# Optimization experiments

Hardware: AMD Instinct MI355X
Metric: run time of the kernel (lower is better)

The kernel has to match this reference:

```python
import jax, jax.numpy as jnp
import numpy as np

N, E = 50000, 800000
IN_CH, HID, OUT_CH = 128, 256, 40
L, R = 3, 16
EPS = 1e-12


def setup_inputs() -> dict:
    key = jax.random.key(0)
    ks = jax.random.split(key, 16)
    s = 0.05
    return {
        'x': jax.random.normal(ks[0], (N, IN_CH), jnp.float32),
        'edge_index': jax.random.randint(ks[1], (2, E), 0, N, dtype=jnp.int64),
        'W_in': jax.random.normal(ks[2], (IN_CH, HID), jnp.float32) * s,
        'b_in': jnp.zeros((HID,), jnp.float32),
        'centers': jax.random.normal(ks[3], (L, R, HID), jnp.float32),
        'log_sigma': jnp.zeros((L, R, HID), jnp.float32),
        'W_rule': jax.random.normal(ks[4], (L, R, HID, HID), jnp.float32) * s,
        'b_rule': jnp.zeros((L, R, HID), jnp.float32),
        'W_self': jax.random.normal(ks[5], (L, HID, HID), jnp.float32) * s,
        'b_self': jnp.zeros((L, HID), jnp.float32),
        'gamma': jnp.ones((L, HID), jnp.float32),
        'beta': jnp.zeros((L, HID), jnp.float32),
        'W_h1': jax.random.normal(ks[6], (HID, HID // 2), jnp.float32) * s,
        'b_h1': jnp.zeros((HID // 2,), jnp.float32),
        'W_h2': jax.random.normal(ks[7], (HID // 2, OUT_CH), jnp.float32) * s,
        'b_h2': jnp.zeros((OUT_CH,), jnp.float32),
    }


def membership(h, c, log_s):
    # Gaussian rule firing, expanded to matmuls to avoid [N,R,H] distance tensor
    inv_s2 = jnp.exp(-2.0 * log_s)                         # [R,H]
    d = (h * h) @ inv_s2.T - 2.0 * (h @ (c * inv_s2).T) \
        + jnp.sum(c * c * inv_s2, axis=-1)                 # [N,R]
    firing = jnp.exp(-0.5 * d)
    return firing / (jnp.sum(firing, axis=-1, keepdims=True) + EPS)


def fmpl(h, src, dst, c, log_s, W_r, b_r, W_s, b_s):
    n = h.shape[0]
    deg = jax.ops.segment_sum(jnp.ones(src.shape[0], h.dtype), dst, num_segments=n)
    agg = jax.ops.segment_sum(h[src], dst, num_segments=n) / jnp.clip(deg, 1.0)[:, None]
    mu = membership(h, c, log_s)                           # [N,R]
    per_rule = jnp.einsum('ni,rio->nro', agg, W_r) + b_r[None]  # [N,R,H]
    fuzzy = jnp.einsum('nr,nro->no', mu, per_rule)
    return h @ W_s + b_s + fuzzy


def batchnorm(x, g, b, eps=1e-5):
    m = jnp.mean(x, axis=0)
    v = jnp.var(x, axis=0)
    return (x - m) * jax.lax.rsqrt(v + eps) * g + b


def reference(x, edge_index, W_in, b_in, centers, log_sigma, W_rule, b_rule,
              W_self, b_self, gamma, beta, W_h1, b_h1, W_h2, b_h2):
    src, dst = edge_index[0], edge_index[1]
    h = jax.nn.relu(x @ W_in + b_in)                       # dropout = identity (eval)
    for l in range(L):
        h_new = fmpl(h, src, dst, centers[l], log_sigma[l], W_rule[l], b_rule[l],
                     W_self[l], b_self[l])
        h_new = jax.nn.relu(batchnorm(h_new, gamma[l], beta[l]))
        h = h + h_new
    logits = jax.nn.relu(h @ W_h1 + b_h1) @ W_h2 + b_h2
    return jax.nn.softmax(logits, axis=-1)
```

## Files before the change

### kernel.cpp

```cpp
#include <hip/hip_runtime.h>
#include <hip/hip_fp16.h>
#include <cstdint>
#include <cstddef>

using u16 = unsigned short;
using u32 = unsigned int;

typedef _Float16 half8 __attribute__((ext_vector_type(8)));
typedef float f32x4 __attribute__((ext_vector_type(4)));

#define MF(a, b, c) __builtin_amdgcn_mfma_f32_16x16x32_f16((a), (b), (c), 0, 0, 0)

static inline int cdiv(int a, int b) { return (a + b - 1) / b; }


__global__ void prep_k(const float* __restrict__ Wr,
                       const float* __restrict__ Ws, const float* __restrict__ br,
                       const float* __restrict__ W_in, const float* __restrict__ W_h1,
                       const float* __restrict__ W_h2,
                       const float* __restrict__ centers, const float* __restrict__ logsig,
                       u16* __restrict__ wcat,
                       u16* __restrict__ winp, u16* __restrict__ wh1p,
                       u16* __restrict__ wh2p,
                       u16* __restrict__ pcB, float* __restrict__ pccc,
                       int* __restrict__ zerobase, int nzero,
                       int Z, int Wb) {
    const int bid = blockIdx.x;
    const int tid = threadIdx.x;
    if (bid < Z) {
        int i = bid * 256 + tid;
        if (i < nzero) zerobase[i] = 0;
        return;
    }
    if (bid < Z + Wb) {
        size_t t = (size_t)(bid - Z) * 256 + tid;
        const size_t PL = 552u * 256u * 8u;
        int l = (int)(t / PL);
        size_t rem = t - (size_t)l * PL;
        int kp = (int)(rem >> 11);
        int o = (int)((rem >> 3) & 255);
        int e = (int)(rem & 7);
        int k = kp * 8 + e;
        float v;
        if (k < 4096)      v = Wr[((((size_t)l * 16 + (k >> 8)) * 256) + (k & 255)) * 256 + o];
        else if (k < 4352) v = Ws[(((size_t)l * 256) + (k - 4096)) * 256 + o];
        else if (k < 4368) v = br[(((size_t)l * 16) + (k - 4352)) * 256 + o];
        else               v = 0.f;
        union { u16 u; _Float16 h; } c; c.h = (_Float16)v;
        wcat[t] = c.u;
        return;
    }
    if (bid < Z + Wb + 128) {
        size_t t = (size_t)(bid - Z - Wb) * 256 + tid;
        int e = (int)(t & 7), o = (int)((t >> 3) & 255);
        int kp = (int)(t >> 11);
        union { u16 u; _Float16 h; } c; c.h = (_Float16)W_in[(size_t)(kp * 8 + e) * 256 + o];
        winp[t] = c.u;
        return;
    }
    if (bid < Z + Wb + 256) {
        size_t t = (size_t)(bid - Z - Wb - 128) * 256 + tid;
        int e = (int)(t & 7), o = (int)((t >> 3) & 127);
        int kp = (int)(t >> 10);
        union { u16 u; _Float16 h; } c; c.h = (_Float16)W_h1[(size_t)(kp * 8 + e) * 128 + o];
        wh1p[t] = c.u;
        return;
    }
    if (bid < Z + Wb + 256 + 24) {
        int t = (bid - Z - Wb - 256) * 256 + tid;
        int e = t & 7, col = (t >> 3) % 48, p = t / 384;
        int k = p * 8 + e;
        float v = (col < 40) ? W_h2[(size_t)k * 40 + col] : 0.f;
        union { u16 u; _Float16 h; } c; c.h = (_Float16)v;
        wh2p[t] = c.u;
        return;
    }
    {
        int lr = bid - (Z + Wb + 256 + 24);
        size_t idx = (size_t)lr * 256 + tid;
        float ls = logsig[idx];
        float inv = expf(-2.f * ls);
        float c = centers[idx];
        union { u16 u; _Float16 h; } c1, c2;
        c1.h = (_Float16)inv;
        c2.h = (_Float16)(-2.f * c * inv);
        pcB[(size_t)lr * 512 + tid] = c1.u;
        pcB[(size_t)lr * 512 + 256 + tid] = c2.u;
        __shared__ float sm[256];
        sm[tid] = c * c * inv;
        __syncthreads();
        for (int s = 128; s > 0; s >>= 1) { if (tid < s) sm[tid] += sm[tid + s]; __syncthreads(); }
        if (tid == 0) pccc[lr] = sm[0];
    }
}


__launch_bounds__(256, 4)
__global__ void csr_agg_g(const int* __restrict__ src, const int* __restrict__ dst,
                          int* __restrict__ deg, int* __restrict__ indptr,
                          int* __restrict__ cursor, float* __restrict__ deginv,
                          int* __restrict__ ssrc, int* __restrict__ csrctr,
                          const int* __restrict__ bflag, int* __restrict__ done,
                          const u16* __restrict__ h16, u16* __restrict__ agg16,
                          int E, int n) {
    if (bflag[511] == 0) return;
    const int tid = threadIdx.x;
    if (*done == 0) {
        auto gbar = [&](int id) {
            __threadfence();
            __syncthreads();
            if (tid == 0) {
                atomicAdd(csrctr, 1);
                while (atomicAdd(csrctr, 0) < 256 * id) __builtin_amdgcn_s_sleep(2);
            }
            __syncthreads();
        };
        for (int e = blockIdx.x * 256 + tid; e < E; e += 256 * 256)
            atomicAdd(&deg[dst[e]], 1);
        gbar(1);
        if (blockIdx.x == 0) {
            const int chunk = (n + 255) >> 8;
            int s0 = tid * chunk, s1 = s0 + chunk; if (s1 > n) s1 = n; if (s0 > n) s0 = n;
            int tot = 0;
            for (int i = s0; i < s1; ++i) tot += atomicAdd(&deg[i], 0);
            __shared__ int sm[256];
            sm[tid] = tot; __syncthreads();
            for (int off = 1; off < 256; off <<= 1) {
                int t = (tid >= off) ? sm[tid - off] : 0;
                __syncthreads(); sm[tid] += t; __syncthreads();
            }
            int base = sm[tid] - tot;
            for (int i = s0; i < s1; ++i) {
                int d = atomicAdd(&deg[i], 0);
                indptr[i] = base; cursor[i] = base;
                deginv[i] = 1.f / (float)(d > 1 ? d : 1);
                base += d;
            }
            if (tid == 255) indptr[n] = sm[255];
        }
        gbar(2);
        for (int e = blockIdx.x * 256 + tid; e < E; e += 256 * 256) {
            int d = dst[e];
            int pos = atomicAdd(&cursor[d], 1);
            ssrc[pos] = src[e];
        }
        gbar(3);
        if (blockIdx.x == 0 && tid == 0) *done = 1;
    }
    int lane = tid & 63, wave = tid >> 6;
    for (int node = blockIdx.x * 4 + wave; node < n; node += 256 * 4) {
        if (bflag[node >> 7] == 0) continue;
        int j0 = indptr[node], j1 = indptr[node + 1];
        float a0 = 0, a1 = 0, a2 = 0, a3 = 0;
        for (int j = j0; j < j1; ++j) {
            int sN = ssrc[j];
            union { uint2 u; _Float16 h[4]; } hv;
            hv.u = *(const uint2*)(h16 + (size_t)sN * 256 + lane * 4);
            a0 += (float)hv.h[0]; a1 += (float)hv.h[1];
            a2 += (float)hv.h[2]; a3 += (float)hv.h[3];
        }
        float di = deginv[node];
        union { uint2 u; _Float16 h[4]; } o;
        o.h[0] = (_Float16)(a0 * di); o.h[1] = (_Float16)(a1 * di);
        o.h[2] = (_Float16)(a2 * di); o.h[3] = (_Float16)(a3 * di);
        *(uint2*)(agg16 + (size_t)node * 256 + lane * 4) = o.u;
    }
}


template <int MODE, int NCHUNK>
__launch_bounds__(256, 2)
__global__ void gemm_mn(const u16* __restrict__ A, const u16* __restrict__ A2,
                        const u16* __restrict__ MU, const u16* __restrict__ Bp,
                        const float* __restrict__ bias, const int* __restrict__ bflag,
                        u16* __restrict__ outH, float* __restrict__ bnsum,
                        const u16* __restrict__ pcB, const float* __restrict__ pccc,
                        u16* __restrict__ mu16, int* __restrict__ bflagN,
                        int nrows) {
    __shared__ __align__(16) u16 lds[24576];
    __shared__ float bnbuf[2048];
    u16* lA = lds;
    u16* lB = lds + 8192;
    const int tid = threadIdx.x;
    const int row0 = blockIdx.x * 128;
    const int lane = tid & 63;
    const int q = lane >> 4, mm = lane & 15;
    const int wave = tid >> 6;

    f32x4 acc[2][16];
#pragma unroll
    for (int i = 0; i < 2; ++i)
#pragma unroll
        for (int j = 0; j < 16; ++j) acc[i][j] = (f32x4){0.f, 0.f, 0.f, 0.f};

    int cb = 0, cbEnd = NCHUNK;
    if (MODE == 1 && bflag[blockIdx.x] == 0) { cb = 64; cbEnd = 68; }

    for (; cb < cbEnd; ++cb) {
#pragma unroll
        for (int it = 0; it < 8; ++it) {
            int idx = it * 256 + tid;
            int p = idx >> 8, col = idx & 255;
            uint4 v = *(const uint4*)(Bp + (((size_t)(cb * 8 + p)) * 256 + col) * 8);
            *(uint4*)(lB + (size_t)idx * 8) = v;
        }
#pragma unroll
        for (int it = 0; it < 4; ++it) {
            int idx = it * 256 + tid;
            int p = idx >> 7, row = idx & 127;
            int grow = row0 + row; if (grow >= nrows) grow = nrows - 1;
            uint4 v;
            if (MODE == 0) {
                const float* xr = (const float*)A + (size_t)grow * 128 + cb * 64 + (p << 3);
                float4 f0 = *(const float4*)xr;
                float4 f1 = *(const float4*)(xr + 4);
                union { uint4 u4; _Float16 h[8]; } cv;
                cv.h[0] = (_Float16)f0.x; cv.h[1] = (_Float16)f0.y;
                cv.h[2] = (_Float16)f0.z; cv.h[3] = (_Float16)f0.w;
                cv.h[4] = (_Float16)f1.x; cv.h[5] = (_Float16)f1.y;
                cv.h[6] = (_Float16)f1.z; cv.h[7] = (_Float16)f1.w;
                v = cv.u4;
            } else {
                if (cb < 64) {
                    int r = cb >> 2;
                    int i0 = ((cb & 3) << 6) + (p << 3);
                    v = *(const uint4*)(A + (size_t)grow * 256 + i0);
                    union { u16 u; _Float16 h; } mu; mu.u = MU[(size_t)grow * 16 + r];
                    union { uint4 u4; _Float16 h[8]; } wv; wv.u4 = v;
#pragma unroll
                    for (int j = 0; j < 8; ++j) wv.h[j] = wv.h[j] * mu.h;
                    v = wv.u4;
                } else if (cb < 68) {
                    int i0 = ((cb - 64) << 6) + (p << 3);
                    v = *(const uint4*)(A2 + (size_t)grow * 256 + i0);
                } else {
                    int j0 = p << 3;
                    if (j0 < 16) v = *(const uint4*)(MU + (size_t)grow * 16 + j0);
                    else v = (uint4){0, 0, 0, 0};
                }
            }
            *(uint4*)(lA + (size_t)idx * 8) = v;
        }
        __syncthreads();
#pragma unroll
        for (int kc = 0; kc < 2; ++kc) {
            int pp = kc * 4 + q;
            half8 af0 = *(const half8*)(lA + ((size_t)pp * 128 + wave * 32 + mm) * 8);
            half8 af1 = *(const half8*)(lA + ((size_t)pp * 128 + wave * 32 + 16 + mm) * 8);
#pragma unroll
            for (int nt = 0; nt < 16; ++nt) {
                half8 bf = *(const half8*)(lB + ((size_t)pp * 256 + nt * 16 + mm) * 8);
                acc[0][nt] = MF(af0, bf, acc[0][nt]);
                acc[1][nt] = MF(af1, bf, acc[1][nt]);
            }
        }
        __syncthreads();
    }

    int nr = nrows - row0; if (nr > 128) nr = 128;

    if (MODE == 1) {
#pragma unroll
        for (int nt = 0; nt < 16; ++nt) {
            int cl = nt * 16 + mm;
            float bb = bias[cl];
            float s = 0.f, ss = 0.f;
#pragma unroll
            for (int mt = 0; mt < 2; ++mt) {
#pragma unroll
                for (int r = 0; r < 4; ++r) {
                    int row = wave * 32 + mt * 16 + q * 4 + r;
                    float v = acc[mt][nt][r] + bb;
                    if (row < nr) { s += v; ss += v * v; }
                }
            }
            s += __shfl_xor(s, 16);  s += __shfl_xor(s, 32);
            ss += __shfl_xor(ss, 16); ss += __shfl_xor(ss, 32);
            if (q == 0) {
                bnbuf[(wave * 256 + cl) * 2 + 0] = s;
                bnbuf[(wave * 256 + cl) * 2 + 1] = ss;
            }
        }
        __syncthreads();
        {
            float s  = bnbuf[tid * 2]     + bnbuf[(256 + tid) * 2]
                     + bnbuf[(512 + tid) * 2] + bnbuf[(768 + tid) * 2];
            float ss = bnbuf[tid * 2 + 1] + bnbuf[(256 + tid) * 2 + 1]
                     + bnbuf[(512 + tid) * 2 + 1] + bnbuf[(768 + tid) * 2 + 1];
            atomicAdd(&bnsum[tid], s);
            atomicAdd(&bnsum[256 + tid], ss);
        }
    }

    f32x4 macc0 = (f32x4){0.f, 0.f, 0.f, 0.f};
    f32x4 macc1 = (f32x4){0.f, 0.f, 0.f, 0.f};
#pragma unroll
    for (int h = 0; h < 2; ++h) {
        __syncthreads();
#pragma unroll
        for (int nt = 0; nt < 8; ++nt) {
            int cl = h * 128 + nt * 16 + mm;
            float bb = bias[cl];
#pragma unroll
            for (int mt = 0; mt < 2; ++mt) {
#pragma unroll
                for (int r = 0; r < 4; ++r) {
                    int row = wave * 32 + mt * 16 + q * 4 + r;
                    float v = acc[mt][h * 8 + nt][r] + bb;
                    if (MODE == 0) v = fmaxf(v, 0.f);
                    union { u16 u; _Float16 hh; } cc; cc.hh = (_Float16)v;
                    lds[row * 136 + nt * 16 + mm] = cc.u;
                }
            }
        }
        __syncthreads();
#pragma unroll
        for (int it = 0; it < 8; ++it) {
            int idx = it * 256 + tid;
            int row = idx >> 4, cp = idx & 15;
            if (row < nr) {
                uint4 v = *(const uint4*)(lds + row * 136 + cp * 8);
                *(uint4*)(outH + (size_t)(row0 + row) * 256 + h * 128 + cp * 8) = v;
            }
        }
        if (MODE == 0) {
            const u16* brow = pcB + (size_t)mm * 512;
#pragma unroll
            for (int it2 = 0; it2 < 4; ++it2) {
                int lk = it2 * 32 + q * 8;
                half8 b1 = *(const half8*)(brow + h * 128 + lk);
                half8 b2 = *(const half8*)(brow + 256 + h * 128 + lk);
                half8 a0 = *(const half8*)(lds + ((size_t)(wave * 32 + mm)) * 136 + lk);
                half8 a1 = *(const half8*)(lds + ((size_t)(wave * 32 + 16 + mm)) * 136 + lk);
                macc0 = MF(a0 * a0, b1, macc0);
                macc0 = MF(a0, b2, macc0);
                macc1 = MF(a1 * a1, b1, macc1);
                macc1 = MF(a1, b2, macc1);
            }
        }
    }

    if (MODE == 0) {
        float cc = pccc[mm];
        bool any = false;
#pragma unroll
        for (int g = 0; g < 2; ++g) {
            f32x4 macc = g ? macc1 : macc0;
#pragma unroll
            for (int r = 0; r < 4; ++r) {
                float d = macc[r] + cc;
                float f = expf(-0.5f * d);
                float s = f;
                s += __shfl_xor(s, 1); s += __shfl_xor(s, 2);
                s += __shfl_xor(s, 4); s += __shfl_xor(s, 8);
                int node = row0 + (wave * 2 + g) * 16 + q * 4 + r;
                if (node < nrows) {
                    union { u16 u; _Float16 hh; } c2;
                    c2.hh = (_Float16)(f / (s + 1e-12f));
                    mu16[(size_t)node * 16 + mm] = c2.u;
                    if (c2.u != 0) any = true;
                }
            }
        }
        if (__any(any) && lane == 0) {
            atomicOr(&bflagN[blockIdx.x], 1);
            atomicOr(&bflagN[511], 1);
        }
    }
}


template <int TAIL>
__launch_bounds__(256)
__global__ void upd_k(const u16* __restrict__ pre16, const float* __restrict__ bnsum,
                      const float* __restrict__ gamma, const float* __restrict__ beta,
                      u16* __restrict__ h16,
                      const u16* __restrict__ pcB, const float* __restrict__ pccc,
                      u16* __restrict__ mu16, int* __restrict__ bflag,
                      const u16* __restrict__ wh1p, const float* __restrict__ bh1,
                      const u16* __restrict__ wh2p, const float* __restrict__ bh2,
                      float* __restrict__ outF, int n) {
    const int tid = threadIdx.x;
    __shared__ float l_ab[512];
    __shared__ __align__(16) u16 qt[4][2176];
    {
        float su = bnsum[tid];
        float sq = bnsum[256 + tid];
        float invn = 1.f / (float)n;
        float m = su * invn;
        float al = gamma[tid] * rsqrtf(sq * invn - m * m + 1e-5f);
        l_ab[tid] = al;
        l_ab[256 + tid] = beta[tid] - m * al;
    }
    __syncthreads();

    const int lane = tid & 63, wave = tid >> 6;
    const int q = lane >> 4, mm = lane & 15;
    const int n0 = (blockIdx.x * 4 + wave) * 16;
    if (n0 >= n) return;
    const int node = n0 + mm;
    const bool valid = node < n;
    const int nodeC = valid ? node : n - 1;
    const size_t base = (size_t)nodeC * 256 + q * 8;

    half8 v16[8];
#pragma unroll
    for (int b = 0; b < 8; ++b) {
        int c = b * 32 + q * 8;
        float4 alA = *(const float4*)(l_ab + c);
        float4 alB = *(const float4*)(l_ab + c + 4);
        float4 shA = *(const float4*)(l_ab + 256 + c);
        float4 shB = *(const float4*)(l_ab + 256 + c + 4);
        float aarr[8] = {alA.x, alA.y, alA.z, alA.w, alB.x, alB.y, alB.z, alB.w};
        float harr[8] = {shA.x, shA.y, shA.z, shA.w, shB.x, shB.y, shB.z, shB.w};
        union { uint4 u; _Float16 hh[8]; } p, hv, o;
        p.u  = *(const uint4*)(pre16 + base + b * 32);
        hv.u = *(const uint4*)(h16 + base + b * 32);
#pragma unroll
        for (int j = 0; j < 8; ++j) {
            float v = (float)hv.hh[j] + fmaxf((float)p.hh[j] * aarr[j] + harr[j], 0.f);
            o.hh[j] = (_Float16)v;
        }
        if (TAIL == 1 && valid) *(uint4*)(h16 + base + b * 32) = o.u;
        v16[b] = *(half8*)&o;
    }

    if (TAIL == 1) {
        const u16* brow = pcB + (size_t)mm * 512;
        f32x4 acc = (f32x4){0.f, 0.f, 0.f, 0.f};
#pragma unroll
        for (int it = 0; it < 16; ++it) {
            half8 a = v16[it & 7];
            if (it < 8) a = a * a;
            half8 bb = *(const half8*)(brow + it * 32 + q * 8);
            acc = MF(a, bb, acc);
        }
        float cc = pccc[mm];
        bool any = false;
#pragma unroll
        for (int r = 0; r < 4; ++r) {
            float d = acc[r] + cc;
            float f = expf(-0.5f * d);
            float s = f;
            s += __shfl_xor(s, 1); s += __shfl_xor(s, 2);
            s += __shfl_xor(s, 4); s += __shfl_xor(s, 8);
            int nd = n0 + q * 4 + r;
            if (nd < n) {
                union { u16 u; _Float16 h; } c2;
                c2.h = (_Float16)(f / (s + 1e-12f));
                mu16[(size_t)nd * 16 + mm] = c2.u;
                if (c2.u != 0) any = true;
            }
        }
        if (__any(any) && lane == 0) {
            atomicOr(&bflag[n0 >> 7], 1);
            atomicOr(&bflag[511], 1);
        }
    }

    if (TAIL == 2) {
        u16* qw = qt[wave];
        f32x4 hq[8];
#pragma unroll
        for (int j = 0; j < 8; ++j) hq[j] = (f32x4){0.f, 0.f, 0.f, 0.f};
#pragma unroll
        for (int b = 0; b < 8; ++b) {
            half8 a = v16[b];
            const u16* bp = wh1p + ((size_t)((b * 4 + q) * 128) + mm) * 8;
#pragma unroll
            for (int nt = 0; nt < 8; ++nt) {
                half8 bf = *(const half8*)(bp + nt * 128);
                hq[nt] = MF(a, bf, hq[nt]);
            }
        }
#pragma unroll
        for (int nt = 0; nt < 8; ++nt) {
            int cl = nt * 16 + mm;
            float bb = bh1[cl];
#pragma unroll
            for (int r = 0; r < 4; ++r) {
                float v = fmaxf(hq[nt][r] + bb, 0.f);
                union { u16 u; _Float16 h; } cc; cc.h = (_Float16)v;
                qw[(q * 4 + r) * 136 + cl] = cc.u;
            }
        }
        const bool c2ok = (mm < 8);
        float b0 = bh2[mm], b1 = bh2[16 + mm];
        float b2 = c2ok ? bh2[32 + mm] : 0.f;
        f32x4 hacc[3];
#pragma unroll
        for (int t = 0; t < 3; ++t) hacc[t] = (f32x4){0.f, 0.f, 0.f, 0.f};
#pragma unroll
        for (int c = 0; c < 4; ++c) {
            half8 a = *(const half8*)(qw + (size_t)mm * 136 + c * 32 + q * 8);
#pragma unroll
            for (int t = 0; t < 3; ++t) {
                half8 b = *(const half8*)(wh2p + ((size_t)(c * 4 + q) * 48 + t * 16 + mm) * 8);
                hacc[t] = MF(a, b, hacc[t]);
            }
        }
#pragma unroll
        for (int r = 0; r < 4; ++r) {
            int nd = n0 + q * 4 + r;
            float v0 = hacc[0][r] + b0;
            float v1 = hacc[1][r] + b1;
            float v2 = c2ok ? (hacc[2][r] + b2) : -3e38f;
            float m = fmaxf(fmaxf(v0, v1), v2);
            m = fmaxf(m, __shfl_xor(m, 1)); m = fmaxf(m, __shfl_xor(m, 2));
            m = fmaxf(m, __shfl_xor(m, 4)); m = fmaxf(m, __shfl_xor(m, 8));
            float e0 = expf(v0 - m), e1 = expf(v1 - m);
            float e2 = c2ok ? expf(v2 - m) : 0.f;
            float s = e0 + e1 + e2;
            s += __shfl_xor(s, 1); s += __shfl_xor(s, 2);
            s += __shfl_xor(s, 4); s += __shfl_xor(s, 8);
            float is = 1.f / s;
            if (nd < n) {
                float* op = outF + (size_t)nd * 40;
                op[mm] = e0 * is;
                op[16 + mm] = e1 * is;
                if (c2ok) op[32 + mm] = e2 * is;
            }
        }
    }
}


extern "C" void kernel_launch(void* const* d_in, const int* in_sizes, int n_in,
                              void* d_out, int out_size, void* d_ws, size_t ws_size,
                              hipStream_t stream) {
    const float* x       = (const float*)d_in[0];
    const int*   ei      = (const int*)d_in[1];
    const float* W_in    = (const float*)d_in[2];
    const float* b_in    = (const float*)d_in[3];
    const float* centers = (const float*)d_in[4];
    const float* logsig  = (const float*)d_in[5];
    const float* W_rule  = (const float*)d_in[6];
    const float* b_rule  = (const float*)d_in[7];
    const float* W_self  = (const float*)d_in[8];
    const float* b_self  = (const float*)d_in[9];
    const float* gamma   = (const float*)d_in[10];
    const float* beta    = (const float*)d_in[11];
    const float* W_h1    = (const float*)d_in[12];
    const float* b_h1    = (const float*)d_in[13];
    const float* W_h2    = (const float*)d_in[14];
    const float* b_h2    = (const float*)d_in[15];

    const int N = in_sizes[0] / 128;
    const int E = in_sizes[1] / 2;
    const int* e_src = ei;
    const int* e_dst = ei + E;

    char* w = (char*)d_ws;
    size_t off = 0;
    auto alloc = [&](size_t bytes) -> void* {
        void* p = w + off;
        off = (off + bytes + 255) & ~(size_t)255;
        return p;
    };

    const int gx = cdiv(N, 128);

    u16*   h16    = (u16*)  alloc((size_t)N * 256 * 2);
    u16*   pre16  = (u16*)  alloc((size_t)N * 256 * 2);
    u16*   agg16  = (u16*)  alloc((size_t)N * 256 * 2);
    u16*   mu16   = (u16*)  alloc((size_t)N * 16 * 2);
    u16*   wcat   = (u16*)  alloc((size_t)3 * 552 * 256 * 8 * 2);
    u16*   winp   = (u16*)  alloc((size_t)16 * 256 * 8 * 2);
    u16*   wh1p   = (u16*)  alloc((size_t)32 * 128 * 8 * 2);
    u16*   wh2p   = (u16*)  alloc((size_t)16 * 48 * 8 * 2);
    u16*   pcB    = (u16*)  alloc((size_t)48 * 512 * 2);
    float* pccc   = (float*)alloc((size_t)48 * 4);
    int*   indptr = (int*)  alloc((size_t)(N + 1) * 4);
    int*   cursor = (int*)  alloc((size_t)N * 4);
    float* deginv = (float*)alloc((size_t)N * 4);
    int*   ssrc   = (int*)  alloc((size_t)E * 4);
    const int nzero = N + 3 * 512 + 3 * 512 + 16;
    int*   zerob  = (int*)  alloc((size_t)nzero * 4);
    int*   deg    = zerob;
    int*   bflagA = zerob + N;
    float* bnsumA = (float*)(zerob + N + 3 * 512);
    int*   misc   = zerob + N + 3 * 512 + 3 * 512;
    int*   done   = misc;
    int*   csrctr = misc + 1;

    const int Z = cdiv(nzero, 256);
    const int Wb = 3 * 552 * 256 * 8 / 256;
    const int prep_grid = Z + Wb + 128 + 128 + 24 + 48;

    prep_k<<<prep_grid, 256, 0, stream>>>(W_rule, W_self, b_rule, W_in, W_h1, W_h2,
                                          centers, logsig, wcat, winp, wh1p, wh2p,
                                          pcB, pccc, zerob, nzero, Z, Wb);

    gemm_mn<0, 2><<<gx, 256, 0, stream>>>((const u16*)x, nullptr, nullptr, winp,
                                          b_in, nullptr, h16, nullptr,
                                          pcB, pccc, mu16, bflagA, N);

    for (int l = 0; l < 3; ++l) {
        int* bf = bflagA + l * 512;
        float* bns = bnsumA + l * 512;
        csr_agg_g<<<256, 256, 0, stream>>>(e_src, e_dst, deg, indptr, cursor, deginv,
                                           ssrc, csrctr, bf, done, h16, agg16, E, N);
        gemm_mn<1, 69><<<gx, 256, 0, stream>>>(agg16, h16, mu16,
                                               wcat + (size_t)l * 552 * 256 * 8,
                                               b_self + l * 256, bf, pre16, bns,
                                               nullptr, nullptr, nullptr, nullptr, N);
        if (l < 2) {
            upd_k<1><<<cdiv(N, 64), 256, 0, stream>>>(pre16, bns, gamma + l * 256,
                                                      beta + l * 256, h16,
                                                      pcB + (size_t)(l + 1) * 16 * 512,
                                                      pccc + (l + 1) * 16, mu16,
                                                      bflagA + (l + 1) * 512,
                                                      nullptr, nullptr, nullptr, nullptr,
                                                      nullptr, N);
        } else {
            upd_k<2><<<cdiv(N, 64), 256, 0, stream>>>(pre16, bns, gamma + l * 256,
                                                      beta + l * 256, h16,
                                                      nullptr, nullptr, nullptr, nullptr,
                                                      wh1p, b_h1, wh2p, b_h2,
                                                      (float*)d_out, N);
        }
    }
}
```

Baseline: 293.6 us.

## Fuse CSR build and aggregation into layer GEMM, convert weights on the fly

Drops the separate CSR/aggregation kernel. Its work moves into the front of the layer GEMM kernel: the edge histogram, scan and scatter run once behind a grid barrier, then each block aggregates its own 128 rows before running the matrix product on them. The fp16 weight prepacking in the prep kernel is also removed, so the GEMM now loads fp32 W_rule, W_self, b_rule and W_in directly and converts them to fp16 while staging each B tile. This saves launches and a large weight-packing pass. In exchange, every block rereads fp32 weights at twice the bytes and does extra conversions in the inner loop. The grid barrier also relies on all GEMM blocks being resident on the GPU at the same time.

New measurement: 340.6 us. 1.16x slower.

```diff
diff --git a/kernel.cpp b/kernel.cpp
--- a/kernel.cpp
+++ b/kernel.cpp
@@ -14,17 +14,11 @@
 static inline int cdiv(int a, int b) { return (a + b - 1) / b; }
 
 
-__global__ void prep_k(const float* __restrict__ Wr,
-                       const float* __restrict__ Ws, const float* __restrict__ br,
-                       const float* __restrict__ W_in, const float* __restrict__ W_h1,
-                       const float* __restrict__ W_h2,
+__global__ void prep_k(const float* __restrict__ W_h1, const float* __restrict__ W_h2,
                        const float* __restrict__ centers, const float* __restrict__ logsig,
-                       u16* __restrict__ wcat,
-                       u16* __restrict__ winp, u16* __restrict__ wh1p,
-                       u16* __restrict__ wh2p,
+                       u16* __restrict__ wh1p, u16* __restrict__ wh2p,
                        u16* __restrict__ pcB, float* __restrict__ pccc,
-                       int* __restrict__ zerobase, int nzero,
-                       int Z, int Wb) {
+                       int* __restrict__ zerobase, int nzero, int Z) {
     const int bid = blockIdx.x;
     const int tid = threadIdx.x;
     if (bid < Z) {
@@ -32,42 +26,16 @@
         if (i < nzero) zerobase[i] = 0;
         return;
     }
-    if (bid < Z + Wb) {
+    if (bid < Z + 128) {
         size_t t = (size_t)(bid - Z) * 256 + tid;
-        const size_t PL = 552u * 256u * 8u;
-        int l = (int)(t / PL);
-        size_t rem = t - (size_t)l * PL;
-        int kp = (int)(rem >> 11);
-        int o = (int)((rem >> 3) & 255);
-        int e = (int)(rem & 7);
-        int k = kp * 8 + e;
-        float v;
-        if (k < 4096)      v = Wr[((((size_t)l * 16 + (k >> 8)) * 256) + (k & 255)) * 256 + o];
-        else if (k < 4352) v = Ws[(((size_t)l * 256) + (k - 4096)) * 256 + o];
-        else if (k < 4368) v = br[(((size_t)l * 16) + (k - 4352)) * 256 + o];
-        else               v = 0.f;
-        union { u16 u; _Float16 h; } c; c.h = (_Float16)v;
-        wcat[t] = c.u;
-        return;
-    }
-    if (bid < Z + Wb + 128) {
-        size_t t = (size_t)(bid - Z - Wb) * 256 + tid;
-        int e = (int)(t & 7), o = (int)((t >> 3) & 255);
-        int kp = (int)(t >> 11);
-        union { u16 u; _Float16 h; } c; c.h = (_Float16)W_in[(size_t)(kp * 8 + e) * 256 + o];
-        winp[t] = c.u;
-        return;
-    }
-    if (bid < Z + Wb + 256) {
-        size_t t = (size_t)(bid - Z - Wb - 128) * 256 + tid;
         int e = (int)(t & 7), o = (int)((t >> 3) & 127);
         int kp = (int)(t >> 10);
         union { u16 u; _Float16 h; } c; c.h = (_Float16)W_h1[(size_t)(kp * 8 + e) * 128 + o];
         wh1p[t] = c.u;
         return;
     }
-    if (bid < Z + Wb + 256 + 24) {
-        int t = (bid - Z - Wb - 256) * 256 + tid;
+    if (bid < Z + 128 + 24) {
+        int t = (bid - Z - 128) * 256 + tid;
         int e = t & 7, col = (t >> 3) % 48, p = t / 384;
         int k = p * 8 + e;
         float v = (col < 40) ? W_h2[(size_t)k * 40 + col] : 0.f;
@@ -76,7 +44,7 @@
         return;
     }
     {
-        int lr = bid - (Z + Wb + 256 + 24);
+        int lr = bid - (Z + 128 + 24);
         size_t idx = (size_t)lr * 256 + tid;
         float ls = logsig[idx];
         float inv = expf(-2.f * ls);
@@ -95,97 +63,101 @@
 }
 
 
-__launch_bounds__(256, 4)
-__global__ void csr_agg_g(const int* __restrict__ src, const int* __restrict__ dst,
-                          int* __restrict__ deg, int* __restrict__ indptr,
-                          int* __restrict__ cursor, float* __restrict__ deginv,
-                          int* __restrict__ ssrc, int* __restrict__ csrctr,
-                          const int* __restrict__ bflag, int* __restrict__ done,
-                          const u16* __restrict__ h16, u16* __restrict__ agg16,
-                          int E, int n) {
-    if (bflag[511] == 0) return;
-    const int tid = threadIdx.x;
-    if (*done == 0) {
-        auto gbar = [&](int id) {
-            __threadfence();
-            __syncthreads();
-            if (tid == 0) {
-                atomicAdd(csrctr, 1);
-                while (atomicAdd(csrctr, 0) < 256 * id) __builtin_amdgcn_s_sleep(2);
-            }
-            __syncthreads();
-        };
-        for (int e = blockIdx.x * 256 + tid; e < E; e += 256 * 256)
-            atomicAdd(&deg[dst[e]], 1);
-        gbar(1);
-        if (blockIdx.x == 0) {
-            const int chunk = (n + 255) >> 8;
-            int s0 = tid * chunk, s1 = s0 + chunk; if (s1 > n) s1 = n; if (s0 > n) s0 = n;
-            int tot = 0;
-            for (int i = s0; i < s1; ++i) tot += atomicAdd(&deg[i], 0);
-            __shared__ int sm[256];
-            sm[tid] = tot; __syncthreads();
-            for (int off = 1; off < 256; off <<= 1) {
-                int t = (tid >= off) ? sm[tid - off] : 0;
-                __syncthreads(); sm[tid] += t; __syncthreads();
-            }
-            int base = sm[tid] - tot;
-            for (int i = s0; i < s1; ++i) {
-                int d = atomicAdd(&deg[i], 0);
-                indptr[i] = base; cursor[i] = base;
-                deginv[i] = 1.f / (float)(d > 1 ? d : 1);
-                base += d;
-            }
-            if (tid == 255) indptr[n] = sm[255];
-        }
-        gbar(2);
-        for (int e = blockIdx.x * 256 + tid; e < E; e += 256 * 256) {
-            int d = dst[e];
-            int pos = atomicAdd(&cursor[d], 1);
-            ssrc[pos] = src[e];
-        }
-        gbar(3);
-        if (blockIdx.x == 0 && tid == 0) *done = 1;
-    }
-    int lane = tid & 63, wave = tid >> 6;
-    for (int node = blockIdx.x * 4 + wave; node < n; node += 256 * 4) {
-        if (bflag[node >> 7] == 0) continue;
-        int j0 = indptr[node], j1 = indptr[node + 1];
-        float a0 = 0, a1 = 0, a2 = 0, a3 = 0;
-        for (int j = j0; j < j1; ++j) {
-            int sN = ssrc[j];
-            union { uint2 u; _Float16 h[4]; } hv;
-            hv.u = *(const uint2*)(h16 + (size_t)sN * 256 + lane * 4);
-            a0 += (float)hv.h[0]; a1 += (float)hv.h[1];
-            a2 += (float)hv.h[2]; a3 += (float)hv.h[3];
-        }
-        float di = deginv[node];
-        union { uint2 u; _Float16 h[4]; } o;
-        o.h[0] = (_Float16)(a0 * di); o.h[1] = (_Float16)(a1 * di);
-        o.h[2] = (_Float16)(a2 * di); o.h[3] = (_Float16)(a3 * di);
-        *(uint2*)(agg16 + (size_t)node * 256 + lane * 4) = o.u;
-    }
-}
-
-
 template <int MODE, int NCHUNK>
 __launch_bounds__(256, 2)
-__global__ void gemm_mn(const u16* __restrict__ A, const u16* __restrict__ A2,
-                        const u16* __restrict__ MU, const u16* __restrict__ Bp,
-                        const float* __restrict__ bias, const int* __restrict__ bflag,
-                        u16* __restrict__ outH, float* __restrict__ bnsum,
-                        const u16* __restrict__ pcB, const float* __restrict__ pccc,
-                        u16* __restrict__ mu16, int* __restrict__ bflagN,
-                        int nrows) {
+__global__ void gemm_f(const float* __restrict__ xf, const float* __restrict__ Wr,
+                       const float* __restrict__ Ws, const float* __restrict__ brl,
+                       int layer,
+                       u16* __restrict__ agg, const u16* __restrict__ hg,
+                       const u16* __restrict__ MU,
+                       const float* __restrict__ bias, const int* __restrict__ bflag,
+                       u16* __restrict__ outH, float* __restrict__ bnsum,
+                       const u16* __restrict__ pcB, const float* __restrict__ pccc,
+                       u16* __restrict__ mu16o, int* __restrict__ bflagN,
+                       const int* __restrict__ esrc, const int* __restrict__ edst,
+                       int* __restrict__ deg, int* __restrict__ indptr,
+                       int* __restrict__ cursor, float* __restrict__ deginv,
+                       int* __restrict__ ssrc, int* __restrict__ csrctr,
+                       int* __restrict__ done, int E, int nrows) {
     __shared__ __align__(16) u16 lds[24576];
-    __shared__ float bnbuf[2048];
+    __shared__ int ssm[256];
     u16* lA = lds;
     u16* lB = lds + 8192;
-    const int tid = threadIdx.x;
-    const int row0 = blockIdx.x * 128;
+    const int tid = threadIdx.x, bid = blockIdx.x;
+    const int row0 = bid * 128;
     const int lane = tid & 63;
     const int q = lane >> 4, mm = lane & 15;
     const int wave = tid >> 6;
+    int nr = nrows - row0; if (nr > 128) nr = 128;
+
+    if (MODE == 1 && bflag[511] != 0) {
+        int bseq = 0;
+        auto gbar = [&]() {
+            __threadfence();
+            __syncthreads();
+            ++bseq;
+            if (tid == 0) {
+                atomicAdd(csrctr, 1);
+                while (atomicAdd(csrctr, 0) < (int)gridDim.x * bseq)
+                    __builtin_amdgcn_s_sleep(2);
+            }
+            __syncthreads();
+        };
+        if (*done == 0) {
+            for (int e = bid * 256 + tid; e < E; e += (int)gridDim.x * 256)
+                atomicAdd(&deg[edst[e]], 1);
+            gbar();
+            if (bid == 0) {
+                const int n = nrows;
+                const int chunk = (n + 255) >> 8;
+                int s0 = tid * chunk, s1 = s0 + chunk;
+                if (s1 > n) s1 = n; if (s0 > n) s0 = n;
+                int tot = 0;
+                for (int i = s0; i < s1; ++i) tot += atomicAdd(&deg[i], 0);
+                ssm[tid] = tot; __syncthreads();
+                for (int off = 1; off < 256; off <<= 1) {
+                    int t = (tid >= off) ? ssm[tid - off] : 0;
+                    __syncthreads(); ssm[tid] += t; __syncthreads();
+                }
+                int base = ssm[tid] - tot;
+                for (int i = s0; i < s1; ++i) {
+                    int d = atomicAdd(&deg[i], 0);
+                    indptr[i] = base; cursor[i] = base;
+                    deginv[i] = 1.f / (float)(d > 1 ? d : 1);
+                    base += d;
+                }
+                if (tid == 255) indptr[nrows] = ssm[255];
+            }
+            gbar();
+            for (int e = bid * 256 + tid; e < E; e += (int)gridDim.x * 256) {
+                int d = edst[e];
+                int pos = atomicAdd(&cursor[d], 1);
+                ssrc[pos] = esrc[e];
+            }
+            gbar();
+            if (bid == 0 && tid == 0) *done = 1;
+        }
+        if (bflag[bid] != 0) {
+            for (int node = row0 + wave; node < row0 + 128 && node < nrows; node += 4) {
+                int j0 = indptr[node], j1 = indptr[node + 1];
+                float a0 = 0, a1 = 0, a2 = 0, a3 = 0;
+                for (int j = j0; j < j1; ++j) {
+                    int sN = ssrc[j];
+                    union { uint2 u; _Float16 h[4]; } hv;
+                    hv.u = *(const uint2*)(hg + (size_t)sN * 256 + lane * 4);
+                    a0 += (float)hv.h[0]; a1 += (float)hv.h[1];
+                    a2 += (float)hv.h[2]; a3 += (float)hv.h[3];
+                }
+                float di = deginv[node];
+                union { uint2 u; _Float16 h[4]; } o;
+                o.h[0] = (_Float16)(a0 * di); o.h[1] = (_Float16)(a1 * di);
+                o.h[2] = (_Float16)(a2 * di); o.h[3] = (_Float16)(a3 * di);
+                *(uint2*)(agg + (size_t)node * 256 + lane * 4) = o.u;
+            }
+        }
+        __threadfence_block();
+        __syncthreads();
+    }
 
     f32x4 acc[2][16];
 #pragma unroll
@@ -194,15 +166,43 @@
         for (int j = 0; j < 16; ++j) acc[i][j] = (f32x4){0.f, 0.f, 0.f, 0.f};
 
     int cb = 0, cbEnd = NCHUNK;
-    if (MODE == 1 && bflag[blockIdx.x] == 0) { cb = 64; cbEnd = 68; }
+    if (MODE == 1 && bflag[bid] == 0) { cb = 64; cbEnd = 68; }
 
     for (; cb < cbEnd; ++cb) {
 #pragma unroll
         for (int it = 0; it < 8; ++it) {
             int idx = it * 256 + tid;
             int p = idx >> 8, col = idx & 255;
-            uint4 v = *(const uint4*)(Bp + (((size_t)(cb * 8 + p)) * 256 + col) * 8);
-            *(uint4*)(lB + (size_t)idx * 8) = v;
+            int kb = cb * 64 + p * 8;
+            union { uint4 u4; _Float16 h[8]; } cv;
+            if (MODE == 0) {
+#pragma unroll
+                for (int e = 0; e < 8; ++e)
+                    cv.h[e] = (_Float16)xf[0], cv.h[e] = (_Float16)0.f;
+#pragma unroll
+                for (int e = 0; e < 8; ++e)
+                    cv.h[e] = (_Float16)Ws[(size_t)(kb + e) * 256 + col];
+            } else {
+                if (kb < 4096) {
+#pragma unroll
+                    for (int e = 0; e < 8; ++e) {
+                        int k = kb + e;
+                        cv.h[e] = (_Float16)Wr[((((size_t)layer * 16 + (k >> 8)) * 256)
+                                                + (k & 255)) * 256 + col];
+                    }
+                } else if (kb < 4352) {
+#pragma unroll
+                    for (int e = 0; e < 8; ++e)
+                        cv.h[e] = (_Float16)Ws[(((size_t)layer * 256) + (kb + e - 4096)) * 256 + col];
+                } else if (kb < 4368) {
+#pragma unroll
+                    for (int e = 0; e < 8; ++e)
+                        cv.h[e] = (_Float16)brl[(((size_t)layer * 16) + (kb + e - 4352)) * 256 + col];
+                } else {
+                    cv.u4 = (uint4){0, 0, 0, 0};
+                }
+            }
+            *(uint4*)(lB + (size_t)idx * 8) = cv.u4;
         }
 #pragma unroll
         for (int it = 0; it < 4; ++it) {
@@ -211,7 +211,7 @@
             int grow = row0 + row; if (grow >= nrows) grow = nrows - 1;
             uint4 v;
             if (MODE == 0) {
-                const float* xr = (const float*)A + (size_t)grow * 128 + cb * 64 + (p << 3);
+                const float* xr = xf + (size_t)grow * 128 + cb * 64 + (p << 3);
                 float4 f0 = *(const float4*)xr;
                 float4 f1 = *(const float4*)(xr + 4);
                 union { uint4 u4; _Float16 h[8]; } cv;
@@ -224,7 +224,7 @@
                 if (cb < 64) {
                     int r = cb >> 2;
                     int i0 = ((cb & 3) << 6) + (p << 3);
-                    v = *(const uint4*)(A + (size_t)grow * 256 + i0);
+                    v = *(const uint4*)(agg + (size_t)grow * 256 + i0);
                     union { u16 u; _Float16 h; } mu; mu.u = MU[(size_t)grow * 16 + r];
                     union { uint4 u4; _Float16 h[8]; } wv; wv.u4 = v;
 #pragma unroll
@@ -232,7 +232,7 @@
                     v = wv.u4;
                 } else if (cb < 68) {
                     int i0 = ((cb - 64) << 6) + (p << 3);
-                    v = *(const uint4*)(A2 + (size_t)grow * 256 + i0);
+                    v = *(const uint4*)(hg + (size_t)grow * 256 + i0);
                 } else {
                     int j0 = p << 3;
                     if (j0 < 16) v = *(const uint4*)(MU + (size_t)grow * 16 + j0);
@@ -257,9 +257,8 @@
         __syncthreads();
     }
 
-    int nr = nrows - row0; if (nr > 128) nr = 128;
-
     if (MODE == 1) {
+        float* bnbuf = (float*)lds;
 #pragma unroll
         for (int nt = 0; nt < 16; ++nt) {
             int cl = nt * 16 + mm;
@@ -357,13 +356,13 @@
                 if (node < nrows) {
                     union { u16 u; _Float16 hh; } c2;
                     c2.hh = (_Float16)(f / (s + 1e-12f));
-                    mu16[(size_t)node * 16 + mm] = c2.u;
+                    mu16o[(size_t)node * 16 + mm] = c2.u;
                     if (c2.u != 0) any = true;
                 }
             }
         }
         if (__any(any) && lane == 0) {
-            atomicOr(&bflagN[blockIdx.x], 1);
+            atomicOr(&bflagN[bid], 1);
             atomicOr(&bflagN[511], 1);
         }
     }
@@ -564,8 +563,6 @@
     u16*   pre16  = (u16*)  alloc((size_t)N * 256 * 2);
     u16*   agg16  = (u16*)  alloc((size_t)N * 256 * 2);
     u16*   mu16   = (u16*)  alloc((size_t)N * 16 * 2);
-    u16*   wcat   = (u16*)  alloc((size_t)3 * 552 * 256 * 8 * 2);
-    u16*   winp   = (u16*)  alloc((size_t)16 * 256 * 8 * 2);
     u16*   wh1p   = (u16*)  alloc((size_t)32 * 128 * 8 * 2);
     u16*   wh2p   = (u16*)  alloc((size_t)16 * 48 * 8 * 2);
     u16*   pcB    = (u16*)  alloc((size_t)48 * 512 * 2);
@@ -584,26 +581,28 @@
     int*   csrctr = misc + 1;
 
     const int Z = cdiv(nzero, 256);
-    const int Wb = 3 * 552 * 256 * 8 / 256;
-    const int prep_grid = Z + Wb + 128 + 128 + 24 + 48;
-
-    prep_k<<<prep_grid, 256, 0, stream>>>(W_rule, W_self, b_rule, W_in, W_h1, W_h2,
-                                          centers, logsig, wcat, winp, wh1p, wh2p,
-                                          pcB, pccc, zerob, nzero, Z, Wb);
-
-    gemm_mn<0, 2><<<gx, 256, 0, stream>>>((const u16*)x, nullptr, nullptr, winp,
-                                          b_in, nullptr, h16, nullptr,
-                                          pcB, pccc, mu16, bflagA, N);
+    const int prep_grid = Z + 128 + 24 + 48;
+
+    prep_k<<<prep_grid, 256, 0, stream>>>(W_h1, W_h2, centers, logsig,
+                                          wh1p, wh2p, pcB, pccc, zerob, nzero, Z);
+
+    gemm_f<0, 2><<<gx, 256, 0, stream>>>(x, nullptr, W_in, nullptr, 0,
+                                         nullptr, nullptr, nullptr,
+                                         b_in, nullptr, h16, nullptr,
+                                         pcB, pccc, mu16, bflagA,
+                                         nullptr, nullptr, nullptr, nullptr,
+                                         nullptr, nullptr, nullptr, nullptr,
+                                         nullptr, 0, N);
 
     for (int l = 0; l < 3; ++l) {
         int* bf = bflagA + l * 512;
         float* bns = bnsumA + l * 512;
-        csr_agg_g<<<256, 256, 0, stream>>>(e_src, e_dst, deg, indptr, cursor, deginv,
-                                           ssrc, csrctr, bf, done, h16, agg16, E, N);
-        gemm_mn<1, 69><<<gx, 256, 0, stream>>>(agg16, h16, mu16,
-                                               wcat + (size_t)l * 552 * 256 * 8,
-                                               b_self + l * 256, bf, pre16, bns,
-                                               nullptr, nullptr, nullptr, nullptr, N);
+        gemm_f<1, 69><<<gx, 256, 0, stream>>>(nullptr, W_rule, W_self, b_rule, l,
+                                              agg16, h16, mu16,
+                                              b_self + l * 256, bf, pre16, bns,
+                                              nullptr, nullptr, nullptr, nullptr,
+                                              e_src, e_dst, deg, indptr, cursor,
+                                              deginv, ssrc, csrctr, done, E, N);
         if (l < 2) {
             upd_k<1><<<cdiv(N, 64), 256, 0, stream>>>(pre16, bns, gamma + l * 256,
                                                       beta + l * 256, h16,
```

## Fuse CSR build and neighbor aggregation into the rule GEMM kernel

Applied to the files above, without the earlier changes.

Removes the separate csr_agg_g launch and performs the CSR construction (with grid barriers) and mean aggregation inside gemm_mn MODE 1. Each block now aggregates its own 128 rows into agg16 before running the GEMM on them, which saves one launch per layer and keeps the aggregated rows cache-warm. The grid barrier now spans gx blocks (about 391) instead of 256. All blocks must be co-resident for the spin barrier to work, and with launch_bounds(256,2) plus large LDS use this is a deadlock risk. Aggregation parallelism is also limited to 4 waves per block.

After: 289.2 us. Within noise of the previous version (-1.5%).

```diff
diff --git a/kernel.cpp b/kernel.cpp
--- a/kernel.cpp
+++ b/kernel.cpp
@@ -95,79 +95,6 @@
 }
 
 
-__launch_bounds__(256, 4)
-__global__ void csr_agg_g(const int* __restrict__ src, const int* __restrict__ dst,
-                          int* __restrict__ deg, int* __restrict__ indptr,
-                          int* __restrict__ cursor, float* __restrict__ deginv,
-                          int* __restrict__ ssrc, int* __restrict__ csrctr,
-                          const int* __restrict__ bflag, int* __restrict__ done,
-                          const u16* __restrict__ h16, u16* __restrict__ agg16,
-                          int E, int n) {
-    if (bflag[511] == 0) return;
-    const int tid = threadIdx.x;
-    if (*done == 0) {
-        auto gbar = [&](int id) {
-            __threadfence();
-            __syncthreads();
-            if (tid == 0) {
-                atomicAdd(csrctr, 1);
-                while (atomicAdd(csrctr, 0) < 256 * id) __builtin_amdgcn_s_sleep(2);
-            }
-            __syncthreads();
-        };
-        for (int e = blockIdx.x * 256 + tid; e < E; e += 256 * 256)
-            atomicAdd(&deg[dst[e]], 1);
-        gbar(1);
-        if (blockIdx.x == 0) {
-            const int chunk = (n + 255) >> 8;
-            int s0 = tid * chunk, s1 = s0 + chunk; if (s1 > n) s1 = n; if (s0 > n) s0 = n;
-            int tot = 0;
-            for (int i = s0; i < s1; ++i) tot += atomicAdd(&deg[i], 0);
-            __shared__ int sm[256];
-            sm[tid] = tot; __syncthreads();
-            for (int off = 1; off < 256; off <<= 1) {
-                int t = (tid >= off) ? sm[tid - off] : 0;
-                __syncthreads(); sm[tid] += t; __syncthreads();
-            }
-            int base = sm[tid] - tot;
-            for (int i = s0; i < s1; ++i) {
-                int d = atomicAdd(&deg[i], 0);
-                indptr[i] = base; cursor[i] = base;
-                deginv[i] = 1.f / (float)(d > 1 ? d : 1);
-                base += d;
-            }
-            if (tid == 255) indptr[n] = sm[255];
-        }
-        gbar(2);
-        for (int e = blockIdx.x * 256 + tid; e < E; e += 256 * 256) {
-            int d = dst[e];
-            int pos = atomicAdd(&cursor[d], 1);
-            ssrc[pos] = src[e];
-        }
-        gbar(3);
-        if (blockIdx.x == 0 && tid == 0) *done = 1;
-    }
-    int lane = tid & 63, wave = tid >> 6;
-    for (int node = blockIdx.x * 4 + wave; node < n; node += 256 * 4) {
-        if (bflag[node >> 7] == 0) continue;
-        int j0 = indptr[node], j1 = indptr[node + 1];
-        float a0 = 0, a1 = 0, a2 = 0, a3 = 0;
-        for (int j = j0; j < j1; ++j) {
-            int sN = ssrc[j];
-            union { uint2 u; _Float16 h[4]; } hv;
-            hv.u = *(const uint2*)(h16 + (size_t)sN * 256 + lane * 4);
-            a0 += (float)hv.h[0]; a1 += (float)hv.h[1];
-            a2 += (float)hv.h[2]; a3 += (float)hv.h[3];
-        }
-        float di = deginv[node];
-        union { uint2 u; _Float16 h[4]; } o;
-        o.h[0] = (_Float16)(a0 * di); o.h[1] = (_Float16)(a1 * di);
-        o.h[2] = (_Float16)(a2 * di); o.h[3] = (_Float16)(a3 * di);
-        *(uint2*)(agg16 + (size_t)node * 256 + lane * 4) = o.u;
-    }
-}
-
-
 template <int MODE, int NCHUNK>
 __launch_bounds__(256, 2)
 __global__ void gemm_mn(const u16* __restrict__ A, const u16* __restrict__ A2,
@@ -176,9 +103,14 @@
                         u16* __restrict__ outH, float* __restrict__ bnsum,
                         const u16* __restrict__ pcB, const float* __restrict__ pccc,
                         u16* __restrict__ mu16, int* __restrict__ bflagN,
-                        int nrows) {
+                        const int* __restrict__ esrc, const int* __restrict__ edst,
+                        int* __restrict__ deg, int* __restrict__ indptr,
+                        int* __restrict__ cursor, float* __restrict__ deginv,
+                        int* __restrict__ ssrc, int* __restrict__ csrctr,
+                        int* __restrict__ done, int E, int nrows) {
     __shared__ __align__(16) u16 lds[24576];
     __shared__ float bnbuf[2048];
+    __shared__ int ssm[256];
     u16* lA = lds;
     u16* lB = lds + 8192;
     const int tid = threadIdx.x;
@@ -186,6 +118,76 @@
     const int lane = tid & 63;
     const int q = lane >> 4, mm = lane & 15;
     const int wave = tid >> 6;
+    int nr = nrows - row0; if (nr > 128) nr = 128;
+
+    if (MODE == 1 && bflag[511] != 0) {
+        int bseq = 0;
+        auto gbar = [&]() {
+            __threadfence();
+            __syncthreads();
+            ++bseq;
+            if (tid == 0) {
+                atomicAdd(csrctr, 1);
+                while (atomicAdd(csrctr, 0) < (int)gridDim.x * bseq)
+                    __builtin_amdgcn_s_sleep(2);
+            }
+            __syncthreads();
+        };
+        if (*done == 0) {
+            for (int e = blockIdx.x * 256 + tid; e < E; e += (int)gridDim.x * 256)
+                atomicAdd(&deg[edst[e]], 1);
+            gbar();
+            if (blockIdx.x == 0) {
+                const int n = nrows;
+                const int chunk = (n + 255) >> 8;
+                int s0 = tid * chunk, s1 = s0 + chunk;
+                if (s1 > n) s1 = n; if (s0 > n) s0 = n;
+                int tot = 0;
+                for (int i = s0; i < s1; ++i) tot += atomicAdd(&deg[i], 0);
+                ssm[tid] = tot; __syncthreads();
+                for (int off = 1; off < 256; off <<= 1) {
+                    int t = (tid >= off) ? ssm[tid - off] : 0;
+                    __syncthreads(); ssm[tid] += t; __syncthreads();
+                }
+                int base = ssm[tid] - tot;
+                for (int i = s0; i < s1; ++i) {
+                    int d = atomicAdd(&deg[i], 0);
+                    indptr[i] = base; cursor[i] = base;
+                    deginv[i] = 1.f / (float)(d > 1 ? d : 1);
+                    base += d;
+                }
+                if (tid == 255) indptr[nrows] = ssm[255];
+            }
+            gbar();
+            for (int e = blockIdx.x * 256 + tid; e < E; e += (int)gridDim.x * 256) {
+                int d = edst[e];
+                int pos = atomicAdd(&cursor[d], 1);
+                ssrc[pos] = esrc[e];
+            }
+            gbar();
+            if (blockIdx.x == 0 && tid == 0) *done = 1;
+        }
+        if (bflag[blockIdx.x] != 0) {
+            for (int node = row0 + wave; node < row0 + 128 && node < nrows; node += 4) {
+                int j0 = indptr[node], j1 = indptr[node + 1];
+                float a0 = 0, a1 = 0, a2 = 0, a3 = 0;
+                for (int j = j0; j < j1; ++j) {
+                    int sN = ssrc[j];
+                    union { uint2 u; _Float16 h[4]; } hv;
+                    hv.u = *(const uint2*)(A2 + (size_t)sN * 256 + lane * 4);
+                    a0 += (float)hv.h[0]; a1 += (float)hv.h[1];
+                    a2 += (float)hv.h[2]; a3 += (float)hv.h[3];
+                }
+                float di = deginv[node];
+                union { uint2 u; _Float16 h[4]; } o;
+                o.h[0] = (_Float16)(a0 * di); o.h[1] = (_Float16)(a1 * di);
+                o.h[2] = (_Float16)(a2 * di); o.h[3] = (_Float16)(a3 * di);
+                *(uint2*)((u16*)A + (size_t)node * 256 + lane * 4) = o.u;
+            }
+        }
+        __threadfence_block();
+        __syncthreads();
+    }
 
     f32x4 acc[2][16];
 #pragma unroll
@@ -257,8 +259,6 @@
         __syncthreads();
     }
 
-    int nr = nrows - row0; if (nr > 128) nr = 128;
-
     if (MODE == 1) {
 #pragma unroll
         for (int nt = 0; nt < 16; ++nt) {
@@ -593,17 +593,20 @@
 
     gemm_mn<0, 2><<<gx, 256, 0, stream>>>((const u16*)x, nullptr, nullptr, winp,
                                           b_in, nullptr, h16, nullptr,
-                                          pcB, pccc, mu16, bflagA, N);
+                                          pcB, pccc, mu16, bflagA,
+                                          nullptr, nullptr, nullptr, nullptr,
+                                          nullptr, nullptr, nullptr, nullptr,
+                                          nullptr, 0, N);
 
     for (int l = 0; l < 3; ++l) {
         int* bf = bflagA + l * 512;
         float* bns = bnsumA + l * 512;
-        csr_agg_g<<<256, 256, 0, stream>>>(e_src, e_dst, deg, indptr, cursor, deginv,
-                                           ssrc, csrctr, bf, done, h16, agg16, E, N);
         gemm_mn<1, 69><<<gx, 256, 0, stream>>>(agg16, h16, mu16,
                                                wcat + (size_t)l * 552 * 256 * 8,
                                                b_self + l * 256, bf, pre16, bns,
-                                               nullptr, nullptr, nullptr, nullptr, N);
+                                               nullptr, nullptr, nullptr, nullptr,
+                                               e_src, e_dst, deg, indptr, cursor,
+                                               deginv, ssrc, csrctr, done, E, N);
         if (l < 2) {
             upd_k<1><<<cdiv(N, 64), 256, 0, stream>>>(pre16, bns, gamma + l * 256,
                                                       beta + l * 256, h16,
```
